# Kernel optimization log

Measured on AMD Instinct MI355X. Metric: run time of the kernel, lower is better.

The kernel has to match this reference:

```python
import jax, jax.numpy as jnp
import numpy as np

P = 7            # pooling_size
SCALE = 1.0 / 16  # spatial_scale


def _roi_align(feat, tf):
    # feat: [B,C,T,H,W] (L2-normalized), tf: [N,7] = [b, x1, y1, t1, x2, y2, t2]
    # RoIAlignAvg with temporal pooled size == T (identity in time): bilinear
    # sample at each spatial bin center for every frame.
    H, W = feat.shape[-2], feat.shape[-1]
    b = tf[:, 0].astype(jnp.int32)
    x1, y1 = tf[:, 1] * SCALE, tf[:, 2] * SCALE
    x2, y2 = tf[:, 4] * SCALE, tf[:, 5] * SCALE
    bw = jnp.maximum(x2 - x1 + SCALE, 1e-3) / P
    bh = jnp.maximum(y2 - y1 + SCALE, 1e-3) / P
    ctr = jnp.arange(P, dtype=feat.dtype) + 0.5
    xs = jnp.clip(x1[:, None] + ctr * bw[:, None], 0.0, W - 1)  # [N,P]
    ys = jnp.clip(y1[:, None] + ctr * bh[:, None], 0.0, H - 1)  # [N,P]
    x0 = jnp.floor(xs); y0 = jnp.floor(ys)
    fx = xs - x0; fy = ys - y0
    x0i = x0.astype(jnp.int32); x1i = jnp.minimum(x0i + 1, W - 1)
    y0i = y0.astype(jnp.int32); y1i = jnp.minimum(y0i + 1, H - 1)

    def g(yi, xi):
        # advanced indices broadcast to [N,P,P]; result [N,P,P,C,T]
        return feat[b[:, None, None], :, :, yi[:, :, None], xi[:, None, :]]

    wy0 = (1 - fy)[:, :, None, None, None]; wy1 = fy[:, :, None, None, None]
    wx0 = (1 - fx)[:, None, :, None, None]; wx1 = fx[:, None, :, None, None]
    out = (wy0 * wx0 * g(y0i, x0i) + wy0 * wx1 * g(y0i, x1i)
           + wy1 * wx0 * g(y1i, x0i) + wy1 * wx1 * g(y1i, x1i))
    return jnp.transpose(out, (0, 3, 4, 1, 2))  # [N,C,T,P,P]


def _forward(base_feat, tubes, gt_rois, gt_tubes, conv_w, conv_b, w1, b1, w2, b2, wp, bp):
    B, C, T = base_feat.shape[:3]
    R = tubes.shape[1]
    # F.normalize(base_feat, p=2, dim=1)
    feat = base_feat / jnp.maximum(
        jnp.linalg.norm(base_feat, axis=1, keepdims=True), 1e-12)

    # --- ragged scatter: rois[b,i,t1:t2+1,1:] = tubes[b,i,[1,2,4,5]] ---
    f = jnp.arange(T)
    f_off = (f[None, :] + jnp.arange(B)[:, None] * T).astype(tubes.dtype)  # [B,T]
    t1 = tubes[..., 3].astype(jnp.int32)[..., None]
    t2 = tubes[..., 6].astype(jnp.int32)[..., None]
    mask = (f[None, None, :] >= t1) & (f[None, None, :] <= t2)  # [B,R,T]
    box = tubes[..., jnp.array([1, 2, 4, 5])]                   # [B,R,4]
    rois_box = jnp.where(mask[..., None], box[:, :, None, :],
                         jnp.zeros((), tubes.dtype))
    rois = jnp.concatenate(
        [jnp.broadcast_to(f_off[:, None, :, None], (B, R, T, 1)), rois_box], -1)

    # --- RoIAlign + AvgPool3d over T + head (eval mode: dropout = identity) ---
    pooled = _roi_align(feat, tubes.reshape(-1, 7))  # [N,C,T,P,P]
    pooled = pooled.mean(axis=2)                     # [N,C,P,P]
    x = jnp.einsum('nchw,oc->nohw', pooled, conv_w) + conv_b[None, :, None, None]
    x = x.reshape(x.shape[0], -1)                    # [N, C*P*P]
    x = jax.nn.relu(x @ w1 + b1)
    x = jax.nn.relu(x @ w2 + b2)
    bbox_pred = x @ wp + bp                          # [N, 4*T]
    return bbox_pred, pooled, rois


def setup_inputs() -> dict:
    B, R, T, C, HF, IMG = 4, 64, 16, 256, 14, 224
    ks = jax.random.split(jax.random.key(0), 16)
    base_feat = jax.random.normal(ks[0], (B, C, T, HF, HF), jnp.float32)
    x1 = jax.random.uniform(ks[1], (B, R), minval=0.0, maxval=IMG / 2)
    y1 = jax.random.uniform(ks[2], (B, R), minval=0.0, maxval=IMG / 2)
    x2 = jnp.minimum(x1 + jax.random.uniform(ks[3], (B, R), minval=16.0, maxval=IMG / 2), IMG - 1.0)
    y2 = jnp.minimum(y1 + jax.random.uniform(ks[4], (B, R), minval=16.0, maxval=IMG / 2), IMG - 1.0)
    tt = jax.random.randint(ks[5], (B, R, 2), 0, T)
    t1 = jnp.min(tt, -1).astype(jnp.float32)
    t2 = jnp.max(tt, -1).astype(jnp.float32)
    bidx = jnp.broadcast_to(jnp.arange(B)[:, None], (B, R)).astype(jnp.float32)
    tubes = jnp.stack([bidx, x1, y1, t1, x2, y2, t2], -1)
    s = 0.02
    return {
        'base_feat': base_feat,
        'tubes': tubes,
        'gt_rois': jax.random.normal(ks[6], (B, 10, T, 5), jnp.float32),
        'gt_tubes': jax.random.normal(ks[7], (B, 10, 7), jnp.float32),
        'conv_w': jax.random.normal(ks[8], (C, C), jnp.float32) * s,
        'conv_b': jnp.zeros((C,), jnp.float32),
        'w1': jax.random.normal(ks[9], (C * P * P, 2048), jnp.float32) * s,
        'b1': jnp.zeros((2048,), jnp.float32),
        'w2': jax.random.normal(ks[10], (2048, 512), jnp.float32) * s,
        'b2': jnp.zeros((512,), jnp.float32),
        'wp': jax.random.normal(ks[11], (512, 4 * T), jnp.float32) * s,
        'bp': jnp.zeros((4 * T,), jnp.float32),
    }


def reference(base_feat, tubes, gt_rois, gt_tubes, conv_w, conv_b, w1, b1, w2, b2, wp, bp):
    return _forward(base_feat, tubes, gt_rois, gt_tubes, conv_w, conv_b, w1, b1, w2, b2, wp, bp)
```

## Files before the change

### kernel.cpp

```cpp
#include <hip/hip_runtime.h>

#define HH 14
#define WW 14
#define HWSZ 196
#define TT 16
#define CC 256
#define BB 4
#define RR 64
#define NROI 256
#define PP 7
#define PP2 49

typedef short s4v __attribute__((ext_vector_type(4)));
typedef short s8v __attribute__((ext_vector_type(8)));
typedef float f4v __attribute__((ext_vector_type(4)));

__device__ inline ushort f2bf(float f) {
    union { float f; unsigned u; } v; v.f = f;
    unsigned r = v.u + 0x7fffu + ((v.u >> 16) & 1u);
    return (ushort)(r >> 16);
}

__global__ void k_sumsq(const float* __restrict__ base, float* __restrict__ partial) {
    int blk = blockIdx.x;
    int bt = blk >> 3, cg = blk & 7;
    int hw = threadIdx.x;
    if (hw >= HWSZ) return;
    int b = bt >> 4, t = bt & 15;
    const float* p = base + ((size_t)(b * CC + cg * 32) * TT + t) * HWSZ + hw;
    float s = 0.f;
    #pragma unroll 8
    for (int c = 0; c < 32; ++c) {
        float v = p[(size_t)c * TT * HWSZ];
        s += v * v;
    }
    partial[cg * 12544 + bt * HWSZ + hw] = s;
}

__global__ void k_finish_inv(const float* __restrict__ partial, float* __restrict__ inv) {
    int j = blockIdx.x * 256 + threadIdx.x;
    if (j >= 12544) return;
    float s = 0.f;
    #pragma unroll
    for (int cg = 0; cg < 8; ++cg) s += partial[cg * 12544 + j];
    inv[j] = 1.0f / fmaxf(sqrtf(s), 1e-12f);
}

__global__ void k_tsum(const float* __restrict__ base, const float* __restrict__ inv,
                       float* __restrict__ tsum) {
    int bc = blockIdx.x;
    int hw = threadIdx.x;
    if (hw >= HWSZ) return;
    int b = bc >> 8;
    const float* p = base + (size_t)bc * TT * HWSZ + hw;
    const float* iv = inv + b * TT * HWSZ + hw;
    float s = 0.f;
    #pragma unroll
    for (int t = 0; t < TT; ++t) s += p[t * HWSZ] * iv[t * HWSZ];
    tsum[(size_t)bc * HWSZ + hw] = s;
}

__global__ void k_roialign(const float* __restrict__ tubes, const float* __restrict__ tsum,
                           float* __restrict__ pooled, float* __restrict__ pooledT,
                           float* __restrict__ rois) {
    __shared__ int sx0[PP], sx1[PP], sy0[PP], sy1[PP];
    __shared__ float sfx[PP], sfy[PP];
    __shared__ int sb;
    int n = blockIdx.x;
    int tid = threadIdx.x;
    if (tid < PP) {
        const float* tb = tubes + n * 7;
        float x1 = tb[1] * 0.0625f, y1 = tb[2] * 0.0625f;
        float x2 = tb[4] * 0.0625f, y2 = tb[5] * 0.0625f;
        float bw = fmaxf(x2 - x1 + 0.0625f, 0.001f) * (1.0f / PP);
        float bh = fmaxf(y2 - y1 + 0.0625f, 0.001f) * (1.0f / PP);
        float ctr = tid + 0.5f;
        float xs = fminf(fmaxf(x1 + ctr * bw, 0.f), (float)(WW - 1));
        float ys = fminf(fmaxf(y1 + ctr * bh, 0.f), (float)(HH - 1));
        float x0f = floorf(xs), y0f = floorf(ys);
        int x0 = (int)x0f, y0 = (int)y0f;
        sx0[tid] = x0; sx1[tid] = min(x0 + 1, WW - 1);
        sy0[tid] = y0; sy1[tid] = min(y0 + 1, HH - 1);
        sfx[tid] = xs - x0f; sfy[tid] = ys - y0f;
        if (tid == 0) sb = (int)tb[0];
    }
    if (tid < TT) {
        const float* tb = tubes + n * 7;
        int t1 = (int)tb[3], t2 = (int)tb[6];
        bool m = (tid >= t1) && (tid <= t2);
        int b = n >> 6;
        float* o = rois + ((size_t)n * TT + tid) * 5;
        o[0] = (float)(b * TT + tid);
        o[1] = m ? tb[1] : 0.f;
        o[2] = m ? tb[2] : 0.f;
        o[3] = m ? tb[4] : 0.f;
        o[4] = m ? tb[5] : 0.f;
    }
    __syncthreads();
    const float* tbase = tsum + (size_t)sb * CC * HWSZ;

    for (int idx = tid; idx < CC * PP2; idx += 256) {
        int c = idx / PP2, bin = idx - (idx / PP2) * PP2;
        int py = bin / PP, px = bin - (bin / PP) * PP;
        const float* tp = tbase + (size_t)c * HWSZ;
        float fx = sfx[px], fy = sfy[py];
        int y0 = sy0[py] * WW, y1 = sy1[py] * WW;
        float v00 = tp[y0 + sx0[px]];
        float v01 = tp[y0 + sx1[px]];
        float v10 = tp[y1 + sx0[px]];
        float v11 = tp[y1 + sx1[px]];
        float v = (1.f - fy) * ((1.f - fx) * v00 + fx * v01)
                + fy        * ((1.f - fx) * v10 + fx * v11);
        pooled[(size_t)n * CC * PP2 + idx] = v * (1.0f / TT);
    }
    for (int idx = tid; idx < PP2 * CC; idx += 256) {
        int bin = idx >> 8, c = idx & 255;
        int py = bin / PP, px = bin - (bin / PP) * PP;
        const float* tp = tbase + (size_t)c * HWSZ;
        float fx = sfx[px], fy = sfy[py];
        int y0 = sy0[py] * WW, y1 = sy1[py] * WW;
        float v00 = tp[y0 + sx0[px]];
        float v01 = tp[y0 + sx1[px]];
        float v10 = tp[y1 + sx0[px]];
        float v11 = tp[y1 + sx1[px]];
        float v = (1.f - fy) * ((1.f - fx) * v00 + fx * v01)
                + fy        * ((1.f - fx) * v10 + fx * v11);
        pooledT[((size_t)n * PP2 + bin) * CC + c] = v * (1.0f / TT);
    }
}

__global__ __launch_bounds__(256) void gemm64(const float* __restrict__ A,
                                              const float* __restrict__ B_,
                                              float* __restrict__ Cp,
                                              int M, int N, int K,
                                              int lda, int ldb, int kChunk) {
    __shared__ float As[16][64];
    __shared__ float Bs[16][68];
    int m0 = blockIdx.x * 64, n0 = blockIdx.y * 64;
    int s = blockIdx.z;
    int k0 = s * kChunk, kend = k0 + kChunk;
    int tid = threadIdx.x;
    int am = tid >> 2, ak = (tid & 3) << 2;
    int bk = tid >> 4, bn = (tid & 15) << 2;
    int tm = tid >> 4, tn = tid & 15;
    float acc[4][4] = {};
    const float* Aptr = A + (size_t)(m0 + am) * lda + ak;
    const float* Bptr = B_ + (size_t)bk * ldb + n0 + bn;

    for (int kk = k0; kk < kend; kk += 16) {
        float4 av = *(const float4*)(Aptr + kk);
        float4 bv = *(const float4*)(Bptr + (size_t)kk * ldb);
        __syncthreads();
        As[ak + 0][am] = av.x;
        As[ak + 1][am] = av.y;
        As[ak + 2][am] = av.z;
        As[ak + 3][am] = av.w;
        *(float4*)&Bs[bk][bn] = bv;
        __syncthreads();
        #pragma unroll
        for (int k = 0; k < 16; ++k) {
            float4 a = *(const float4*)&As[k][tm << 2];
            float4 b = *(const float4*)&Bs[k][tn << 2];
            float a4[4] = {a.x, a.y, a.z, a.w};
            float b4[4] = {b.x, b.y, b.z, b.w};
            #pragma unroll
            for (int i = 0; i < 4; ++i)
                #pragma unroll
                for (int j = 0; j < 4; ++j)
                    acc[i][j] += a4[i] * b4[j];
        }
    }
    float* Cs = Cp + (size_t)s * M * N;
    #pragma unroll
    for (int i = 0; i < 4; ++i) {
        float4 v = make_float4(acc[i][0], acc[i][1], acc[i][2], acc[i][3]);
        *(float4*)&Cs[(size_t)(m0 + (tm << 2) + i) * N + n0 + (tn << 2)] = v;
    }
}

__global__ void k_reduce(const float* __restrict__ part, const float* __restrict__ bias,
                         float* __restrict__ out, int MN, int N, int S, int relu) {
    int idx = blockIdx.x * 256 + threadIdx.x;
    if (idx >= MN) return;
    float s = bias[idx % N];
    for (int i = 0; i < S; ++i) s += part[(size_t)i * MN + idx];
    if (relu) s = fmaxf(s, 0.f);
    out[idx] = s;
}

__global__ __launch_bounds__(512) void conv_mfma(const float* __restrict__ pooledT,
                                                 const float* __restrict__ conv_w,
                                                 const float* __restrict__ conv_b,
                                                 ushort* __restrict__ xb) {
    __shared__ __align__(16) ushort Ab[2][8192];
    __shared__ __align__(16) ushort Bres[8192];
    const int m0 = blockIdx.x * 256, o0 = blockIdx.y * 64;
    const int tid = threadIdx.x;
    const int lane = tid & 63, w = tid >> 6;
    const int wm = w & 3, wn = w >> 2;
    const int fr = lane & 15, fg = lane >> 4;

    for (int ii = tid; ii < 2048; ii += 512) {
        int o_l = ii >> 5, cq = ii & 31;
        const float* s = conv_w + (size_t)(o0 + o_l) * 256 + cq * 8;
        float4 v0 = *(const float4*)s;
        float4 v1 = *(const float4*)(s + 4);
        float vv[8] = {v0.x, v0.y, v0.z, v0.w, v1.x, v1.y, v1.z, v1.w};
        int dbase = (cq >> 2) * 2048 + (o_l >> 4) * 512 + (cq & 3) * 128 + (o_l & 15);
        #pragma unroll
        for (int jc = 0; jc < 8; ++jc) Bres[dbase + jc * 16] = f2bf(vv[jc]);
    }

    int ii0 = tid, ii1 = 512 + tid, ii2 = 1024 + tid, ii3 = 1536 + tid;
    const float* pA0 = pooledT + (size_t)(m0 + (ii0 >> 3)) * 256 + (ii0 & 7) * 4;
    const float* pA1 = pooledT + (size_t)(m0 + (ii1 >> 3)) * 256 + (ii1 & 7) * 4;
    const float* pA2 = pooledT + (size_t)(m0 + (ii2 >> 3)) * 256 + (ii2 & 7) * 4;
    const float* pA3 = pooledT + (size_t)(m0 + (ii3 >> 3)) * 256 + (ii3 & 7) * 4;
#define CDOFF(ii) (((ii >> 3) >> 4) * 512 + ((ii & 7) >> 1) * 128 + ((ii >> 3) & 15) * 8 + (ii & 1) * 4)
    const int do0 = CDOFF(ii0), do1 = CDOFF(ii1), do2 = CDOFF(ii2), do3 = CDOFF(ii3);
#undef CDOFF
    float4 a0_, a1_, a2_, a3_;
#define CONV_LOAD(t) do { a0_ = *(const float4*)(pA0 + (t) * 32); \
                          a1_ = *(const float4*)(pA1 + (t) * 32); \
                          a2_ = *(const float4*)(pA2 + (t) * 32); \
                          a3_ = *(const float4*)(pA3 + (t) * 32); } while (0)
#define W4(dst, v) do { s4v _u; _u[0]=(short)f2bf((v).x); _u[1]=(short)f2bf((v).y); \
                        _u[2]=(short)f2bf((v).z); _u[3]=(short)f2bf((v).w); \
                        *(s4v*)(dst) = _u; } while (0)
#define CONV_WRITE(buf) do { W4(Ab[buf] + do0, a0_); W4(Ab[buf] + do1, a1_); \
                             W4(Ab[buf] + do2, a2_); W4(Ab[buf] + do3, a3_); } while (0)

    CONV_LOAD(0);
    CONV_WRITE(0);
    __syncthreads();

    const int aoff = wm * 2048 + fg * 128 + fr * 8;
    f4v acc[4][2];
    #pragma unroll
    for (int i = 0; i < 4; ++i)
        #pragma unroll
        for (int j = 0; j < 2; ++j) acc[i][j] = (f4v){0.f, 0.f, 0.f, 0.f};

    for (int t = 0; t < 8; ++t) {
        if (t < 7) CONV_LOAD(t + 1);
        const ushort* A = Ab[t & 1];
        s8v a0 = *(const s8v*)(A + aoff);
        s8v a1 = *(const s8v*)(A + aoff + 512);
        s8v a2 = *(const s8v*)(A + aoff + 1024);
        s8v a3 = *(const s8v*)(A + aoff + 1536);
        unsigned bbase = (unsigned)(size_t)(&Bres[0]) + t * 4096 + wn * 2048 + fg * 256 + fr * 2;
        s4v bl0, bh0, bl1, bh1;
        asm volatile("ds_read_b64_tr_b16 %0, %2\n\t"
                     "ds_read_b64_tr_b16 %1, %2 offset:128"
                     : "=v"(bl0), "=v"(bh0) : "v"(bbase));
        asm volatile("ds_read_b64_tr_b16 %0, %2 offset:1024\n\t"
                     "ds_read_b64_tr_b16 %1, %2 offset:1152"
                     : "=v"(bl1), "=v"(bh1) : "v"(bbase));
        asm volatile("s_waitcnt lgkmcnt(0)" ::: "memory");
        __builtin_amdgcn_sched_barrier(0);
        s8v b0, b1;
        b0[0] = bl0[0]; b0[1] = bl0[1]; b0[2] = bl0[2]; b0[3] = bl0[3];
        b0[4] = bh0[0]; b0[5] = bh0[1]; b0[6] = bh0[2]; b0[7] = bh0[3];
        b1[0] = bl1[0]; b1[1] = bl1[1]; b1[2] = bl1[2]; b1[3] = bl1[3];
        b1[4] = bh1[0]; b1[5] = bh1[1]; b1[6] = bh1[2]; b1[7] = bh1[3];
        acc[0][0] = __builtin_amdgcn_mfma_f32_16x16x32_bf16(a0, b0, acc[0][0], 0, 0, 0);
        acc[0][1] = __builtin_amdgcn_mfma_f32_16x16x32_bf16(a0, b1, acc[0][1], 0, 0, 0);
        acc[1][0] = __builtin_amdgcn_mfma_f32_16x16x32_bf16(a1, b0, acc[1][0], 0, 0, 0);
        acc[1][1] = __builtin_amdgcn_mfma_f32_16x16x32_bf16(a1, b1, acc[1][1], 0, 0, 0);
        acc[2][0] = __builtin_amdgcn_mfma_f32_16x16x32_bf16(a2, b0, acc[2][0], 0, 0, 0);
        acc[2][1] = __builtin_amdgcn_mfma_f32_16x16x32_bf16(a2, b1, acc[2][1], 0, 0, 0);
        acc[3][0] = __builtin_amdgcn_mfma_f32_16x16x32_bf16(a3, b0, acc[3][0], 0, 0, 0);
        acc[3][1] = __builtin_amdgcn_mfma_f32_16x16x32_bf16(a3, b1, acc[3][1], 0, 0, 0);
        if (t < 7) CONV_WRITE((t + 1) & 1);
        __syncthreads();
    }
#undef CONV_LOAD
#undef CONV_WRITE
#undef W4

    #pragma unroll
    for (int ni = 0; ni < 2; ++ni) {
        int o = o0 + wn * 32 + ni * 16 + fr;
        float cb = conv_b[o];
        int obase = (o >> 5) * 8192 + (((o >> 3) & 3)) * 128 + (o & 7);
        #pragma unroll
        for (int mi = 0; mi < 4; ++mi)
            #pragma unroll
            for (int i = 0; i < 4; ++i) {
                int gm = m0 + wm * 64 + mi * 16 + fg * 4 + i;
                int n = gm / 49, hw = gm - n * 49;
                xb[(size_t)hw * 65536 + obase + (n >> 4) * 512 + (n & 15) * 8]
                    = f2bf(acc[mi][ni][i] + cb);
            }
    }
}

__global__ __launch_bounds__(512) void fc1_mfma(const ushort* __restrict__ xb,
                                                const float* __restrict__ w1,
                                                float* __restrict__ part) {
    __shared__ __align__(16) ushort Ab[4][8192];
    __shared__ __align__(16) ushort Bbf[2][2048];
    const int s = blockIdx.x, nblk = blockIdx.y;
    const int n0 = nblk * 64;
    const int k0 = s * 1568;
    const int tid = threadIdx.x;
    const int lane = tid & 63, w = tid >> 6;
    const int wm = w & 3, wn = w >> 2;
    const int fr = lane & 15, fg = lane >> 4;

    const ushort* gA = xb + (size_t)s * 49 * 8192;
    const int slot0 = tid, slot1 = 512 + tid;

    const int kr = (w >> 2) * 16 + (lane >> 2);
    const int bnb = w & 3, bnq = lane & 3;
    const int ncol = n0 + bnb * 16 + bnq * 4;
    const int bw_u = bnb * 512 + kr * 16 + bnq * 4;

    const int aoff = wm * 2048 + fg * 128 + fr * 8;
    f4v acc[4][2];
    #pragma unroll
    for (int i = 0; i < 4; ++i)
        #pragma unroll
        for (int j = 0; j < 2; ++j) acc[i][j] = (f4v){0.f, 0.f, 0.f, 0.f};

#define STAGE_A(buf, kg) do {                                                                   \
    ushort* _d = Ab[buf];                                                                       \
    __builtin_amdgcn_global_load_lds(                                                           \
        (const __attribute__((address_space(1))) void*)(gA + (size_t)(kg) * 8192 + slot0 * 8),  \
        (__attribute__((address_space(3))) void*)(_d + slot0 * 8), 16, 0, 0);                   \
    __builtin_amdgcn_global_load_lds(                                                           \
        (const __attribute__((address_space(1))) void*)(gA + (size_t)(kg) * 8192 + slot1 * 8),  \
        (__attribute__((address_space(3))) void*)(_d + slot1 * 8), 16, 0, 0);                   \
} while (0)
#define GBP(t) (*(const float4*)(w1 +                                                           \
    (size_t)(((unsigned)(k0 + (t) * 32 + kr) & 255u) * 49 +                                     \
             ((unsigned)(k0 + (t) * 32 + kr) >> 8)) * 2048 + ncol))
#define BWRITE(buf, rb) do {                                                                    \
    s4v _u; _u[0] = (short)f2bf((rb).x); _u[1] = (short)f2bf((rb).y);                           \
    _u[2] = (short)f2bf((rb).z); _u[3] = (short)f2bf((rb).w);                                   \
    *(s4v*)&Bbf[buf][bw_u] = _u;                                                                \
} while (0)

    float4 rb0, rb1, rb2, rb3;
    STAGE_A(0, 0);
    STAGE_A(1, 1);
    rb0 = GBP(0); rb1 = GBP(1); rb2 = GBP(2); rb3 = GBP(3);
    BWRITE(0, rb0);
    __builtin_amdgcn_sched_barrier(0);
    asm volatile("s_waitcnt vmcnt(3) lgkmcnt(0)" ::: "memory");
    __builtin_amdgcn_s_barrier();
    __builtin_amdgcn_sched_barrier(0);

#define FC1_BODY(t, rbL, rbU) do {                                                              \
    int kg2 = (t) + 2 > 48 ? 48 : (t) + 2;                                                      \
    int kg4 = (t) + 4 > 48 ? 48 : (t) + 4;                                                      \
    STAGE_A(((t) + 2) & 3, kg2);                                                                \
    __builtin_amdgcn_sched_barrier(0);                                                          \
    rbL = GBP(kg4);                                                                             \
    __builtin_amdgcn_sched_barrier(0);                                                          \
    const ushort* _A = Ab[(t) & 3];                                                             \
    s8v _a0 = *(const s8v*)(_A + aoff);                                                         \
    s8v _a1 = *(const s8v*)(_A + aoff + 512);                                                   \
    s8v _a2 = *(const s8v*)(_A + aoff + 1024);                                                  \
    s8v _a3 = *(const s8v*)(_A + aoff + 1536);                                                  \
    unsigned _bb = (unsigned)(size_t)(&Bbf[(t) & 1][0]) + wn * 2048 + fg * 256 + fr * 2;        \
    s4v _bl0, _bh0, _bl1, _bh1;                                                                 \
    asm volatile("ds_read_b64_tr_b16 %0, %2\n\t"                                                \
                 "ds_read_b64_tr_b16 %1, %2 offset:128"                                         \
                 : "=v"(_bl0), "=v"(_bh0) : "v"(_bb));                                          \
    asm volatile("ds_read_b64_tr_b16 %0, %2 offset:1024\n\t"                                    \
                 "ds_read_b64_tr_b16 %1, %2 offset:1152"                                        \
                 : "=v"(_bl1), "=v"(_bh1) : "v"(_bb));                                          \
    asm volatile("s_waitcnt lgkmcnt(0)" ::: "memory");                                          \
    __builtin_amdgcn_sched_barrier(0);                                                          \
    s8v _b0, _b1;                                                                               \
    _b0[0]=_bl0[0]; _b0[1]=_bl0[1]; _b0[2]=_bl0[2]; _b0[3]=_bl0[3];                             \
    _b0[4]=_bh0[0]; _b0[5]=_bh0[1]; _b0[6]=_bh0[2]; _b0[7]=_bh0[3];                             \
    _b1[0]=_bl1[0]; _b1[1]=_bl1[1]; _b1[2]=_bl1[2]; _b1[3]=_bl1[3];                             \
    _b1[4]=_bh1[0]; _b1[5]=_bh1[1]; _b1[6]=_bh1[2]; _b1[7]=_bh1[3];                             \
    acc[0][0] = __builtin_amdgcn_mfma_f32_16x16x32_bf16(_a0, _b0, acc[0][0], 0, 0, 0);          \
    acc[0][1] = __builtin_amdgcn_mfma_f32_16x16x32_bf16(_a0, _b1, acc[0][1], 0, 0, 0);          \
    acc[1][0] = __builtin_amdgcn_mfma_f32_16x16x32_bf16(_a1, _b0, acc[1][0], 0, 0, 0);          \
    acc[1][1] = __builtin_amdgcn_mfma_f32_16x16x32_bf16(_a1, _b1, acc[1][1], 0, 0, 0);          \
    acc[2][0] = __builtin_amdgcn_mfma_f32_16x16x32_bf16(_a2, _b0, acc[2][0], 0, 0, 0);          \
    acc[2][1] = __builtin_amdgcn_mfma_f32_16x16x32_bf16(_a2, _b1, acc[2][1], 0, 0, 0);          \
    acc[3][0] = __builtin_amdgcn_mfma_f32_16x16x32_bf16(_a3, _b0, acc[3][0], 0, 0, 0);          \
    acc[3][1] = __builtin_amdgcn_mfma_f32_16x16x32_bf16(_a3, _b1, acc[3][1], 0, 0, 0);          \
    BWRITE(((t) + 1) & 1, rbU);                                                                 \
    __builtin_amdgcn_sched_barrier(0);                                                          \
    asm volatile("s_waitcnt vmcnt(4) lgkmcnt(0)" ::: "memory");                                 \
    __builtin_amdgcn_s_barrier();                                                               \
    __builtin_amdgcn_sched_barrier(0);                                                          \
} while (0)

    for (int tb = 0; tb < 44; tb += 4) {
        FC1_BODY(tb + 0, rb0, rb1);
        FC1_BODY(tb + 1, rb1, rb2);
        FC1_BODY(tb + 2, rb2, rb3);
        FC1_BODY(tb + 3, rb3, rb0);
    }
    FC1_BODY(44, rb0, rb1);
    FC1_BODY(45, rb1, rb2);
    FC1_BODY(46, rb2, rb3);
    FC1_BODY(47, rb3, rb0);

    {
        const ushort* _A = Ab[0];
        s8v _a0 = *(const s8v*)(_A + aoff);
        s8v _a1 = *(const s8v*)(_A + aoff + 512);
        s8v _a2 = *(const s8v*)(_A + aoff + 1024);
        s8v _a3 = *(const s8v*)(_A + aoff + 1536);
        unsigned _bb = (unsigned)(size_t)(&Bbf[0][0]) + wn * 2048 + fg * 256 + fr * 2;
        s4v _bl0, _bh0, _bl1, _bh1;
        asm volatile("ds_read_b64_tr_b16 %0, %2\n\t"
                     "ds_read_b64_tr_b16 %1, %2 offset:128"
                     : "=v"(_bl0), "=v"(_bh0) : "v"(_bb));
        asm volatile("ds_read_b64_tr_b16 %0, %2 offset:1024\n\t"
                     "ds_read_b64_tr_b16 %1, %2 offset:1152"
                     : "=v"(_bl1), "=v"(_bh1) : "v"(_bb));
        asm volatile("s_waitcnt lgkmcnt(0)" ::: "memory");
        __builtin_amdgcn_sched_barrier(0);
        s8v _b0, _b1;
        _b0[0]=_bl0[0]; _b0[1]=_bl0[1]; _b0[2]=_bl0[2]; _b0[3]=_bl0[3];
        _b0[4]=_bh0[0]; _b0[5]=_bh0[1]; _b0[6]=_bh0[2]; _b0[7]=_bh0[3];
        _b1[0]=_bl1[0]; _b1[1]=_bl1[1]; _b1[2]=_bl1[2]; _b1[3]=_bl1[3];
        _b1[4]=_bh1[0]; _b1[5]=_bh1[1]; _b1[6]=_bh1[2]; _b1[7]=_bh1[3];
        acc[0][0] = __builtin_amdgcn_mfma_f32_16x16x32_bf16(_a0, _b0, acc[0][0], 0, 0, 0);
        acc[0][1] = __builtin_amdgcn_mfma_f32_16x16x32_bf16(_a0, _b1, acc[0][1], 0, 0, 0);
        acc[1][0] = __builtin_amdgcn_mfma_f32_16x16x32_bf16(_a1, _b0, acc[1][0], 0, 0, 0);
        acc[1][1] = __builtin_amdgcn_mfma_f32_16x16x32_bf16(_a1, _b1, acc[1][1], 0, 0, 0);
        acc[2][0] = __builtin_amdgcn_mfma_f32_16x16x32_bf16(_a2, _b0, acc[2][0], 0, 0, 0);
        acc[2][1] = __builtin_amdgcn_mfma_f32_16x16x32_bf16(_a2, _b1, acc[2][1], 0, 0, 0);
        acc[3][0] = __builtin_amdgcn_mfma_f32_16x16x32_bf16(_a3, _b0, acc[3][0], 0, 0, 0);
        acc[3][1] = __builtin_amdgcn_mfma_f32_16x16x32_bf16(_a3, _b1, acc[3][1], 0, 0, 0);
    }
#undef FC1_BODY
#undef STAGE_A
#undef GBP
#undef BWRITE

    float* dst = part + (size_t)s * 256 * 2048 + n0 + wn * 32 + fr;
    #pragma unroll
    for (int mi = 0; mi < 4; ++mi)
        #pragma unroll
        for (int ni = 0; ni < 2; ++ni)
            #pragma unroll
            for (int i = 0; i < 4; ++i) {
                int row = wm * 64 + mi * 16 + fg * 4 + i;
                dst[(size_t)row * 2048 + ni * 16] = acc[mi][ni][i];
            }
}

extern "C" void kernel_launch(void* const* d_in, const int* in_sizes, int n_in,
                              void* d_out, int out_size, void* d_ws, size_t ws_size,
                              hipStream_t stream) {
    const float* base   = (const float*)d_in[0];
    const float* tubes  = (const float*)d_in[1];
    const float* conv_w = (const float*)d_in[4];
    const float* conv_b = (const float*)d_in[5];
    const float* w1     = (const float*)d_in[6];
    const float* b1     = (const float*)d_in[7];
    const float* w2     = (const float*)d_in[8];
    const float* b2     = (const float*)d_in[9];
    const float* wp     = (const float*)d_in[10];
    const float* bp     = (const float*)d_in[11];

    float* out    = (float*)d_out;
    float* bbox   = out;
    float* pooled = out + 16384;
    float* rois   = out + 16384 + 3211264;

    float* ws      = (float*)d_ws;
    float* inv     = ws;
    float* partial = ws + 12544;
    float* tsum    = ws + 112896;
    float* pooledT = ws + 313600;
    ushort* xb     = (ushort*)(ws + 3524864);
    float* h1      = ws + 6736128;
    float* h2      = ws + 7260416;
    float* part    = ws + 7391488;

    k_sumsq<<<BB * TT * 8, 256, 0, stream>>>(base, partial);
    k_finish_inv<<<49, 256, 0, stream>>>(partial, inv);
    k_tsum<<<BB * CC, 256, 0, stream>>>(base, inv, tsum);
    k_roialign<<<NROI, 256, 0, stream>>>(tubes, tsum, pooled, pooledT, rois);

    conv_mfma<<<dim3(49, 4), 512, 0, stream>>>(pooledT, conv_w, conv_b, xb);

    fc1_mfma<<<dim3(8, 32), 512, 0, stream>>>(xb, w1, part);
    k_reduce<<<(256 * 2048 + 255) / 256, 256, 0, stream>>>(part, b1, h1, 256 * 2048, 2048, 8, 1);

    gemm64<<<dim3(4, 8, 8), 256, 0, stream>>>(h1, w2, part,
                                              256, 512, 2048, 2048, 512, 256);
    k_reduce<<<(256 * 512 + 255) / 256, 256, 0, stream>>>(part, b2, h2, 256 * 512, 512, 8, 1);

    gemm64<<<dim3(4, 1, 8), 256, 0, stream>>>(h2, wp, part,
                                              256, 64, 512, 512, 64, 64);
    k_reduce<<<(256 * 64 + 255) / 256, 256, 0, stream>>>(part, bp, bbox, 256 * 64, 64, 8, 0);
}
```

Measured before the change: 125.9 us.

## Move fc2 to bf16 MFMA, store split-K partials in bf16, fuse fc3 bias

Replaces the fp32 SIMT gemm64 used for fc2 with a bf16 MFMA kernel that reads a bf16 h1 written directly in MFMA-friendly tiled layout by a new reduce kernel. Split-K partials from fc1 and fc2 are stored as bf16 instead of fp32 to halve reduce traffic, and reduces are vectorized 8-wide. The final small projection becomes a single kernel with bias folded in, removing a gemm plus reduce launch. Risks extra precision loss from bf16 partial sums and h1.

```diff
diff --git a/kernel.cpp b/kernel.cpp
--- a/kernel.cpp
+++ b/kernel.cpp
@@ -19,6 +19,10 @@
     union { float f; unsigned u; } v; v.f = f;
     unsigned r = v.u + 0x7fffu + ((v.u >> 16) & 1u);
     return (ushort)(r >> 16);
+}
+__device__ inline float bf2f(ushort u) {
+    union { unsigned u; float f; } v; v.u = ((unsigned)u) << 16;
+    return v.f;
 }
 
 __global__ void k_sumsq(const float* __restrict__ base, float* __restrict__ partial) {
@@ -127,65 +131,6 @@
                 + fy        * ((1.f - fx) * v10 + fx * v11);
         pooledT[((size_t)n * PP2 + bin) * CC + c] = v * (1.0f / TT);
     }
-}
-
-__global__ __launch_bounds__(256) void gemm64(const float* __restrict__ A,
-                                              const float* __restrict__ B_,
-                                              float* __restrict__ Cp,
-                                              int M, int N, int K,
-                                              int lda, int ldb, int kChunk) {
-    __shared__ float As[16][64];
-    __shared__ float Bs[16][68];
-    int m0 = blockIdx.x * 64, n0 = blockIdx.y * 64;
-    int s = blockIdx.z;
-    int k0 = s * kChunk, kend = k0 + kChunk;
-    int tid = threadIdx.x;
-    int am = tid >> 2, ak = (tid & 3) << 2;
-    int bk = tid >> 4, bn = (tid & 15) << 2;
-    int tm = tid >> 4, tn = tid & 15;
-    float acc[4][4] = {};
-    const float* Aptr = A + (size_t)(m0 + am) * lda + ak;
-    const float* Bptr = B_ + (size_t)bk * ldb + n0 + bn;
-
-    for (int kk = k0; kk < kend; kk += 16) {
-        float4 av = *(const float4*)(Aptr + kk);
-        float4 bv = *(const float4*)(Bptr + (size_t)kk * ldb);
-        __syncthreads();
-        As[ak + 0][am] = av.x;
-        As[ak + 1][am] = av.y;
-        As[ak + 2][am] = av.z;
-        As[ak + 3][am] = av.w;
-        *(float4*)&Bs[bk][bn] = bv;
-        __syncthreads();
-        #pragma unroll
-        for (int k = 0; k < 16; ++k) {
-            float4 a = *(const float4*)&As[k][tm << 2];
-            float4 b = *(const float4*)&Bs[k][tn << 2];
-            float a4[4] = {a.x, a.y, a.z, a.w};
-            float b4[4] = {b.x, b.y, b.z, b.w};
-            #pragma unroll
-            for (int i = 0; i < 4; ++i)
-                #pragma unroll
-                for (int j = 0; j < 4; ++j)
-                    acc[i][j] += a4[i] * b4[j];
-        }
-    }
-    float* Cs = Cp + (size_t)s * M * N;
-    #pragma unroll
-    for (int i = 0; i < 4; ++i) {
-        float4 v = make_float4(acc[i][0], acc[i][1], acc[i][2], acc[i][3]);
-        *(float4*)&Cs[(size_t)(m0 + (tm << 2) + i) * N + n0 + (tn << 2)] = v;
-    }
-}
-
-__global__ void k_reduce(const float* __restrict__ part, const float* __restrict__ bias,
-                         float* __restrict__ out, int MN, int N, int S, int relu) {
-    int idx = blockIdx.x * 256 + threadIdx.x;
-    if (idx >= MN) return;
-    float s = bias[idx % N];
-    for (int i = 0; i < S; ++i) s += part[(size_t)i * MN + idx];
-    if (relu) s = fmaxf(s, 0.f);
-    out[idx] = s;
 }
 
 __global__ __launch_bounds__(512) void conv_mfma(const float* __restrict__ pooledT,
@@ -297,7 +242,7 @@
 
 __global__ __launch_bounds__(512) void fc1_mfma(const ushort* __restrict__ xb,
                                                 const float* __restrict__ w1,
-                                                float* __restrict__ part) {
+                                                ushort* __restrict__ partb) {
     __shared__ __align__(16) ushort Ab[4][8192];
     __shared__ __align__(16) ushort Bbf[2][2048];
     const int s = blockIdx.x, nblk = blockIdx.y;
@@ -393,16 +338,12 @@
     __builtin_amdgcn_sched_barrier(0);                                                          \
 } while (0)
 
-    for (int tb = 0; tb < 44; tb += 4) {
+    for (int tb = 0; tb < 48; tb += 4) {
         FC1_BODY(tb + 0, rb0, rb1);
         FC1_BODY(tb + 1, rb1, rb2);
         FC1_BODY(tb + 2, rb2, rb3);
         FC1_BODY(tb + 3, rb3, rb0);
     }
-    FC1_BODY(44, rb0, rb1);
-    FC1_BODY(45, rb1, rb2);
-    FC1_BODY(46, rb2, rb3);
-    FC1_BODY(47, rb3, rb0);
 
     {
         const ushort* _A = Ab[0];
@@ -439,7 +380,7 @@
 #undef GBP
 #undef BWRITE
 
-    float* dst = part + (size_t)s * 256 * 2048 + n0 + wn * 32 + fr;
+    ushort* dst = partb + (size_t)s * 524288 + n0 + wn * 32 + fr;
     #pragma unroll
     for (int mi = 0; mi < 4; ++mi)
         #pragma unroll
@@ -447,8 +388,205 @@
             #pragma unroll
             for (int i = 0; i < 4; ++i) {
                 int row = wm * 64 + mi * 16 + fg * 4 + i;
-                dst[(size_t)row * 2048 + ni * 16] = acc[mi][ni][i];
+                dst[(size_t)row * 2048 + ni * 16] = f2bf(acc[mi][ni][i]);
             }
+}
+
+__global__ void k_reduce_bf(const ushort* __restrict__ part, const float* __restrict__ bias,
+                            ushort* __restrict__ h1b) {
+    int idx = blockIdx.x * 256 + threadIdx.x;
+    if (idx >= 65536) return;
+    int m = idx >> 8;
+    int ko = idx & 255;
+    int kbase = ko * 8;
+    float s[8];
+    #pragma unroll
+    for (int j = 0; j < 8; ++j) s[j] = bias[kbase + j];
+    #pragma unroll
+    for (int i = 0; i < 8; ++i) {
+        s8v v = *(const s8v*)(part + (size_t)i * 524288 + (size_t)m * 2048 + kbase);
+        #pragma unroll
+        for (int j = 0; j < 8; ++j) s[j] += bf2f((ushort)v[j]);
+    }
+    ushort o[8];
+    #pragma unroll
+    for (int j = 0; j < 8; ++j) o[j] = f2bf(fmaxf(s[j], 0.f));
+    size_t dst = (size_t)(ko >> 2) * 8192 + (m >> 4) * 512 + (ko & 3) * 128 + (m & 15) * 8;
+    *(s8v*)(h1b + dst) = *(s8v*)o;
+}
+
+__global__ __launch_bounds__(512) void fc2_mfma(const ushort* __restrict__ h1b,
+                                                const float* __restrict__ w2,
+                                                ushort* __restrict__ partb2) {
+    __shared__ __align__(16) ushort Bbf[2][2048];
+    const int s = blockIdx.x, nblk = blockIdx.y;
+    const int n0 = nblk * 64;
+    const int k0 = s * 256;
+    const int tid = threadIdx.x;
+    const int lane = tid & 63, w = tid >> 6;
+    const int wm = w & 3, wn = w >> 2;
+    const int fr = lane & 15, fg = lane >> 4;
+
+    const ushort* gA = h1b + (size_t)s * 8 * 8192;
+
+    const int kr = (w >> 2) * 16 + (lane >> 2);
+    const int bnb = w & 3, bnq = lane & 3;
+    const int ncol = n0 + bnb * 16 + bnq * 4;
+    const int bw_u = bnb * 512 + kr * 16 + bnq * 4;
+
+    const int aoff = wm * 2048 + fg * 128 + fr * 8;
+    f4v acc[4][2];
+    #pragma unroll
+    for (int i = 0; i < 4; ++i)
+        #pragma unroll
+        for (int j = 0; j < 2; ++j) acc[i][j] = (f4v){0.f, 0.f, 0.f, 0.f};
+
+#define GBP2(t) (*(const float4*)(w2 + (size_t)(k0 + (t) * 32 + kr) * 512 + ncol))
+#define BWRITE2(buf, rb) do {                                                                   \
+    s4v _u; _u[0] = (short)f2bf((rb).x); _u[1] = (short)f2bf((rb).y);                           \
+    _u[2] = (short)f2bf((rb).z); _u[3] = (short)f2bf((rb).w);                                   \
+    *(s4v*)&Bbf[buf][bw_u] = _u;                                                                \
+} while (0)
+
+    s8v aA0, aA1, aA2, aA3, aB0, aB1, aB2, aB3;
+    float4 rb0, rb1, rb2, rb3;
+
+    aA0 = *(const s8v*)(gA + aoff);
+    aA1 = *(const s8v*)(gA + aoff + 512);
+    aA2 = *(const s8v*)(gA + aoff + 1024);
+    aA3 = *(const s8v*)(gA + aoff + 1536);
+    rb0 = GBP2(0); rb1 = GBP2(1); rb2 = GBP2(2); rb3 = GBP2(3);
+    BWRITE2(0, rb0);
+    __syncthreads();
+
+#define FC2_BODY(t, rbL, rbU, aC0, aC1, aC2, aC3, aN0, aN1, aN2, aN3) do {                      \
+    int kg1 = (t) + 1 > 7 ? 7 : (t) + 1;                                                        \
+    int kg4 = (t) + 4 > 7 ? 7 : (t) + 4;                                                        \
+    const ushort* _gn = gA + (size_t)kg1 * 8192;                                                \
+    aN0 = *(const s8v*)(_gn + aoff);                                                            \
+    aN1 = *(const s8v*)(_gn + aoff + 512);                                                      \
+    aN2 = *(const s8v*)(_gn + aoff + 1024);                                                     \
+    aN3 = *(const s8v*)(_gn + aoff + 1536);                                                     \
+    rbL = GBP2(kg4);                                                                            \
+    unsigned _bb = (unsigned)(size_t)(&Bbf[(t) & 1][0]) + wn * 2048 + fg * 256 + fr * 2;        \
+    s4v _bl0, _bh0, _bl1, _bh1;                                                                 \
+    asm volatile("ds_read_b64_tr_b16 %0, %2\n\t"                                                \
+                 "ds_read_b64_tr_b16 %1, %2 offset:128"                                         \
+                 : "=v"(_bl0), "=v"(_bh0) : "v"(_bb));                                          \
+    asm volatile("ds_read_b64_tr_b16 %0, %2 offset:1024\n\t"                                    \
+                 "ds_read_b64_tr_b16 %1, %2 offset:1152"                                        \
+                 : "=v"(_bl1), "=v"(_bh1) : "v"(_bb));                                          \
+    asm volatile("s_waitcnt lgkmcnt(0)" ::: "memory");                                          \
+    __builtin_amdgcn_sched_barrier(0);                                                          \
+    s8v _b0, _b1;                                                                               \
+    _b0[0]=_bl0[0]; _b0[1]=_bl0[1]; _b0[2]=_bl0[2]; _b0[3]=_bl0[3];                             \
+    _b0[4]=_bh0[0]; _b0[5]=_bh0[1]; _b0[6]=_bh0[2]; _b0[7]=_bh0[3];                             \
+    _b1[0]=_bl1[0]; _b1[1]=_bl1[1]; _b1[2]=_bl1[2]; _b1[3]=_bl1[3];                             \
+    _b1[4]=_bh1[0]; _b1[5]=_bh1[1]; _b1[6]=_bh1[2]; _b1[7]=_bh1[3];                             \
+    acc[0][0] = __builtin_amdgcn_mfma_f32_16x16x32_bf16(aC0, _b0, acc[0][0], 0, 0, 0);          \
+    acc[0][1] = __builtin_amdgcn_mfma_f32_16x16x32_bf16(aC0, _b1, acc[0][1], 0, 0, 0);          \
+    acc[1][0] = __builtin_amdgcn_mfma_f32_16x16x32_bf16(aC1, _b0, acc[1][0], 0, 0, 0);          \
+    acc[1][1] = __builtin_amdgcn_mfma_f32_16x16x32_bf16(aC1, _b1, acc[1][1], 0, 0, 0);          \
+    acc[2][0] = __builtin_amdgcn_mfma_f32_16x16x32_bf16(aC2, _b0, acc[2][0], 0, 0, 0);          \
+    acc[2][1] = __builtin_amdgcn_mfma_f32_16x16x32_bf16(aC2, _b1, acc[2][1], 0, 0, 0);          \
+    acc[3][0] = __builtin_amdgcn_mfma_f32_16x16x32_bf16(aC3, _b0, acc[3][0], 0, 0, 0);          \
+    acc[3][1] = __builtin_amdgcn_mfma_f32_16x16x32_bf16(aC3, _b1, acc[3][1], 0, 0, 0);          \
+    BWRITE2(((t) + 1) & 1, rbU);                                                                \
+    __syncthreads();                                                                            \
+} while (0)
+
+    FC2_BODY(0, rb0, rb1, aA0, aA1, aA2, aA3, aB0, aB1, aB2, aB3);
+    FC2_BODY(1, rb1, rb2, aB0, aB1, aB2, aB3, aA0, aA1, aA2, aA3);
+    FC2_BODY(2, rb2, rb3, aA0, aA1, aA2, aA3, aB0, aB1, aB2, aB3);
+    FC2_BODY(3, rb3, rb0, aB0, aB1, aB2, aB3, aA0, aA1, aA2, aA3);
+    FC2_BODY(4, rb0, rb1, aA0, aA1, aA2, aA3, aB0, aB1, aB2, aB3);
+    FC2_BODY(5, rb1, rb2, aB0, aB1, aB2, aB3, aA0, aA1, aA2, aA3);
+    FC2_BODY(6, rb2, rb3, aA0, aA1, aA2, aA3, aB0, aB1, aB2, aB3);
+
+    {
+        unsigned _bb = (unsigned)(size_t)(&Bbf[1][0]) + wn * 2048 + fg * 256 + fr * 2;
+        s4v _bl0, _bh0, _bl1, _bh1;
+        asm volatile("ds_read_b64_tr_b16 %0, %2\n\t"
+                     "ds_read_b64_tr_b16 %1, %2 offset:128"
+                     : "=v"(_bl0), "=v"(_bh0) : "v"(_bb));
+        asm volatile("ds_read_b64_tr_b16 %0, %2 offset:1024\n\t"
+                     "ds_read_b64_tr_b16 %1, %2 offset:1152"
+                     : "=v"(_bl1), "=v"(_bh1) : "v"(_bb));
+        asm volatile("s_waitcnt lgkmcnt(0)" ::: "memory");
+        __builtin_amdgcn_sched_barrier(0);
+        s8v _b0, _b1;
+        _b0[0]=_bl0[0]; _b0[1]=_bl0[1]; _b0[2]=_bl0[2]; _b0[3]=_bl0[3];
+        _b0[4]=_bh0[0]; _b0[5]=_bh0[1]; _b0[6]=_bh0[2]; _b0[7]=_bh0[3];
+        _b1[0]=_bl1[0]; _b1[1]=_bl1[1]; _b1[2]=_bl1[2]; _b1[3]=_bl1[3];
+        _b1[4]=_bh1[0]; _b1[5]=_bh1[1]; _b1[6]=_bh1[2]; _b1[7]=_bh1[3];
+        acc[0][0] = __builtin_amdgcn_mfma_f32_16x16x32_bf16(aB0, _b0, acc[0][0], 0, 0, 0);
+        acc[0][1] = __builtin_amdgcn_mfma_f32_16x16x32_bf16(aB0, _b1, acc[0][1], 0, 0, 0);
+        acc[1][0] = __builtin_amdgcn_mfma_f32_16x16x32_bf16(aB1, _b0, acc[1][0], 0, 0, 0);
+        acc[1][1] = __builtin_amdgcn_mfma_f32_16x16x32_bf16(aB1, _b1, acc[1][1], 0, 0, 0);
+        acc[2][0] = __builtin_amdgcn_mfma_f32_16x16x32_bf16(aB2, _b0, acc[2][0], 0, 0, 0);
+        acc[2][1] = __builtin_amdgcn_mfma_f32_16x16x32_bf16(aB2, _b1, acc[2][1], 0, 0, 0);
+        acc[3][0] = __builtin_amdgcn_mfma_f32_16x16x32_bf16(aB3, _b0, acc[3][0], 0, 0, 0);
+        acc[3][1] = __builtin_amdgcn_mfma_f32_16x16x32_bf16(aB3, _b1, acc[3][1], 0, 0, 0);
+    }
+#undef FC2_BODY
+#undef GBP2
+#undef BWRITE2
+
+    ushort* dst = partb2 + (size_t)s * 131072 + n0 + wn * 32 + fr;
+    #pragma unroll
+    for (int mi = 0; mi < 4; ++mi)
+        #pragma unroll
+        for (int ni = 0; ni < 2; ++ni)
+            #pragma unroll
+            for (int i = 0; i < 4; ++i) {
+                int row = wm * 64 + mi * 16 + fg * 4 + i;
+                dst[(size_t)row * 512 + ni * 16] = f2bf(acc[mi][ni][i]);
+            }
+}
+
+__global__ void k_reduce_bf2(const ushort* __restrict__ part, const float* __restrict__ bias,
+                             float* __restrict__ h2) {
+    int idx = blockIdx.x * 256 + threadIdx.x;
+    if (idx >= 16384) return;
+    int m = idx >> 6;
+    int no = idx & 63;
+    int nbase = no * 8;
+    float s[8];
+    #pragma unroll
+    for (int j = 0; j < 8; ++j) s[j] = bias[nbase + j];
+    #pragma unroll
+    for (int i = 0; i < 8; ++i) {
+        s8v v = *(const s8v*)(part + (size_t)i * 131072 + (size_t)m * 512 + nbase);
+        #pragma unroll
+        for (int j = 0; j < 8; ++j) s[j] += bf2f((ushort)v[j]);
+    }
+    float* o = h2 + (size_t)m * 512 + nbase;
+    #pragma unroll
+    for (int j = 0; j < 8; ++j) o[j] = fmaxf(s[j], 0.f);
+}
+
+__global__ __launch_bounds__(256) void fc3_small(const float* __restrict__ h2,
+                                                 const float* __restrict__ wp,
+                                                 const float* __restrict__ bp,
+                                                 float* __restrict__ bbox) {
+    __shared__ float sh2[8][512];
+    int blk = blockIdx.x;
+    int tid = threadIdx.x;
+    int n = tid & 63;
+    int mr = tid >> 6;
+    int m0 = blk * 8;
+    for (int i = tid; i < 8 * 512; i += 256)
+        sh2[i >> 9][i & 511] = h2[(size_t)(m0 + (i >> 9)) * 512 + (i & 511)];
+    __syncthreads();
+    float b = bp[n];
+    float acc0 = b, acc1 = b;
+    for (int k = 0; k < 512; ++k) {
+        float wv = wp[k * 64 + n];
+        acc0 += sh2[mr][k] * wv;
+        acc1 += sh2[mr + 4][k] * wv;
+    }
+    bbox[(size_t)(m0 + mr) * 64 + n] = acc0;
+    bbox[(size_t)(m0 + mr + 4) * 64 + n] = acc1;
 }
 
 extern "C" void kernel_launch(void* const* d_in, const int* in_sizes, int n_in,
@@ -476,9 +614,11 @@
     float* tsum    = ws + 112896;
     float* pooledT = ws + 313600;
     ushort* xb     = (ushort*)(ws + 3524864);
-    float* h1      = ws + 6736128;
+    ushort* h1b    = (ushort*)(ws + 6736128);
     float* h2      = ws + 7260416;
     float* part    = ws + 7391488;
+    ushort* partb  = (ushort*)part;
+    ushort* partb2 = (ushort*)(part + 2097152);
 
     k_sumsq<<<BB * TT * 8, 256, 0, stream>>>(base, partial);
     k_finish_inv<<<49, 256, 0, stream>>>(partial, inv);
@@ -487,14 +627,11 @@
 
     conv_mfma<<<dim3(49, 4), 512, 0, stream>>>(pooledT, conv_w, conv_b, xb);
 
-    fc1_mfma<<<dim3(8, 32), 512, 0, stream>>>(xb, w1, part);
-    k_reduce<<<(256 * 2048 + 255) / 256, 256, 0, stream>>>(part, b1, h1, 256 * 2048, 2048, 8, 1);
-
-    gemm64<<<dim3(4, 8, 8), 256, 0, stream>>>(h1, w2, part,
-                                              256, 512, 2048, 2048, 512, 256);
-    k_reduce<<<(256 * 512 + 255) / 256, 256, 0, stream>>>(part, b2, h2, 256 * 512, 512, 8, 1);
-
-    gemm64<<<dim3(4, 1, 8), 256, 0, stream>>>(h2, wp, part,
-                                              256, 64, 512, 512, 64, 64);
-    k_reduce<<<(256 * 64 + 255) / 256, 256, 0, stream>>>(part, bp, bbox, 256 * 64, 64, 8, 0);
-}
+    fc1_mfma<<<dim3(8, 32), 512, 0, stream>>>(xb, w1, partb);
+    k_reduce_bf<<<256, 256, 0, stream>>>(partb, b1, h1b);
+
+    fc2_mfma<<<dim3(8, 8), 512, 0, stream>>>(h1b, w2, partb2);
+    k_reduce_bf2<<<64, 256, 0, stream>>>(partb2, b2, h2);
+
+    fc3_small<<<32, 256, 0, stream>>>(h2, wp, bp, bbox);
+}
```

Measured after the change: 123.1 us. 1.02x faster.
